# Optimization experiments

Measured on AMD Instinct MI355X. Metric: run time of the kernel, lower is better.

The kernel has to match this reference:

```python
import jax, jax.numpy as jnp
import numpy as np

NHEAD = 8
TEMP = 1.0
LAMB = 1.0
G_MIN = 1e-3


def _linear(x, w, b):
    # torch nn.Linear convention: w is (out, in)
    return x @ w.T + b


def _ln(x, s, b):
    m = x.mean(-1, keepdims=True)
    v = ((x - m) ** 2).mean(-1, keepdims=True)
    return (x - m) / jnp.sqrt(v + 1e-5) * s + b


def _gate(x, w, b):
    # UncertaintyGate, gate_mode='mu_times_evi'
    nig = _linear(x, w, b)  # [B, L, 4]
    mu = nig[..., 0]
    v = jax.nn.softplus(nig[..., 1]) + 1e-6
    alpha = jax.nn.softplus(nig[..., 2]) + 1.0 + 1e-6
    beta = jax.nn.softplus(nig[..., 3]) + 1e-6
    sigma_e2 = beta / (v * (alpha - 1.0))
    g = jax.nn.sigmoid(mu) * jnp.exp(-LAMB * sigma_e2)
    return jnp.clip(g, G_MIN, 1.0)  # [B, L]


def _cross_attn(q, k, v, gate, mask):
    B, Lq, D = q.shape
    Lk = k.shape[1]
    hd = D // NHEAD
    q = q.reshape(B, Lq, NHEAD, hd).transpose(0, 2, 1, 3)
    k = k.reshape(B, Lk, NHEAD, hd).transpose(0, 2, 1, 3)
    v = v.reshape(B, Lk, NHEAD, hd).transpose(0, 2, 1, 3)
    scores = jnp.einsum('bhqd,bhkd->bhqk', q, k) / jnp.sqrt(jnp.float32(hd))
    scores = scores + jnp.log(gate + 1e-9)[:, None, None, :]  # per-key log-gate bias
    scores = jnp.where(mask[:, None, None, :] == 0, -1e9, scores)
    attn = jax.nn.softmax(scores / TEMP, axis=-1)
    out = jnp.einsum('bhqk,bhkd->bhqd', attn, v)
    return out.transpose(0, 2, 1, 3).reshape(B, Lq, D)


def _ffn(x, w1, b1, w2, b2):
    return _linear(jax.nn.gelu(_linear(x, w1, b1), approximate=False), w2, b2)


def setup_inputs() -> dict:
    key = jax.random.key(0)
    ks = iter(jax.random.split(key, 64))
    D, B, Ld, Lp = 512, 16, 256, 1024
    def w(shape, s=0.02):
        return jax.random.normal(next(ks), shape, jnp.float32) * s
    inp = {
        'h_d': jax.random.normal(next(ks), (B, Ld, D), jnp.float32),
        'h_p': jax.random.normal(next(ks), (B, Lp, D), jnp.float32),
        'gd_w': w((4, D)), 'gd_b': jnp.zeros((4,), jnp.float32),
        'gp_w': w((4, D)), 'gp_b': jnp.zeros((4,), jnp.float32),
        'wqd_w': w((D, D)), 'wqd_b': jnp.zeros((D,), jnp.float32),
        'wkp_w': w((D, D)), 'wkp_b': jnp.zeros((D,), jnp.float32),
        'wvp_w': w((D, D)), 'wvp_b': jnp.zeros((D,), jnp.float32),
        'wqp_w': w((D, D)), 'wqp_b': jnp.zeros((D,), jnp.float32),
        'wkd_w': w((D, D)), 'wkd_b': jnp.zeros((D,), jnp.float32),
        'wvd_w': w((D, D)), 'wvd_b': jnp.zeros((D,), jnp.float32),
        'od_w': w((D, D)), 'od_b': jnp.zeros((D,), jnp.float32),
        'op_w': w((D, D)), 'op_b': jnp.zeros((D,), jnp.float32),
        'fd1_w': w((4 * D, D)), 'fd1_b': jnp.zeros((4 * D,), jnp.float32),
        'fd2_w': w((D, 4 * D)), 'fd2_b': jnp.zeros((D,), jnp.float32),
        'fp1_w': w((4 * D, D)), 'fp1_b': jnp.zeros((4 * D,), jnp.float32),
        'fp2_w': w((D, 4 * D)), 'fp2_b': jnp.zeros((D,), jnp.float32),
        'nd1_s': jnp.ones((D,), jnp.float32), 'nd1_b': jnp.zeros((D,), jnp.float32),
        'nd2_s': jnp.ones((D,), jnp.float32), 'nd2_b': jnp.zeros((D,), jnp.float32),
        'np1_s': jnp.ones((D,), jnp.float32), 'np1_b': jnp.zeros((D,), jnp.float32),
        'np2_s': jnp.ones((D,), jnp.float32), 'np2_b': jnp.zeros((D,), jnp.float32),
        'mask_d': jnp.ones((B, Ld), jnp.int32),
        'mask_p': jnp.ones((B, Lp), jnp.int32),
    }
    return inp


def reference(h_d, h_p, gd_w, gd_b, gp_w, gp_b, wqd_w, wqd_b, wkp_w, wkp_b,
              wvp_w, wvp_b, wqp_w, wqp_b, wkd_w, wkd_b, wvd_w, wvd_b,
              od_w, od_b, op_w, op_b, fd1_w, fd1_b, fd2_w, fd2_b,
              fp1_w, fp1_b, fp2_w, fp2_b, nd1_s, nd1_b, nd2_s, nd2_b,
              np1_s, np1_b, np2_s, np2_b, mask_d, mask_p):
    # gates are computed from the ORIGINAL inputs
    g_d = _gate(h_d, gd_w, gd_b)
    g_p = _gate(h_p, gp_w, gp_b)
    # drug attends to protein
    attn_d = _cross_attn(_linear(h_d, wqd_w, wqd_b),
                         _linear(h_p, wkp_w, wkp_b),
                         _linear(h_p, wvp_w, wvp_b), g_p, mask_p)
    h_d = _ln(h_d + _linear(attn_d, od_w, od_b), nd1_s, nd1_b)
    # protein attends to UPDATED drug (matches original control flow)
    attn_p = _cross_attn(_linear(h_p, wqp_w, wqp_b),
                         _linear(h_d, wkd_w, wkd_b),
                         _linear(h_d, wvd_w, wvd_b), g_d, mask_d)
    h_p = _ln(h_p + _linear(attn_p, op_w, op_b), np1_s, np1_b)
    h_d = _ln(h_d + _ffn(h_d, fd1_w, fd1_b, fd2_w, fd2_b), nd2_s, nd2_b)
    h_p = _ln(h_p + _ffn(h_p, fp1_w, fp1_b, fp2_w, fp2_b), np2_s, np2_b)
    return (h_d, h_p)
```

## Files before the change

### kernel.cpp

```cpp
#include <hip/hip_runtime.h>

typedef float f32x4 __attribute__((ext_vector_type(4)));
typedef short bfrag __attribute__((ext_vector_type(8)));
typedef short s16x8 __attribute__((ext_vector_type(8)));
typedef unsigned short u16;

__device__ __forceinline__ u16 f2bf(float f) {
  union { float f; unsigned u; } x; x.f = f;
  unsigned r = x.u + 0x7fffu + ((x.u >> 16) & 1u);
  return (u16)(r >> 16);
}
__device__ __forceinline__ float bf2f(u16 v) {
  union { unsigned u; float f; } x; x.u = ((unsigned)v) << 16;
  return x.f;
}

__device__ __forceinline__ void g2l16(const void* g, void* l) {
  void* gnc = const_cast<void*>(g);
  __builtin_amdgcn_global_load_lds((__attribute__((address_space(1))) void*)gnc,
                                   (__attribute__((address_space(3))) void*)l, 16, 0, 0);
}

__device__ __forceinline__ f32x4 mfma16(bfrag a, bfrag b, f32x4 c) {
  asm volatile("v_mfma_f32_16x16x32_bf16 %0, %1, %2, %0" : "+v"(c) : "v"(a), "v"(b));
  return c;
}

__device__ __forceinline__ float wred_sum(float s) {
  #pragma unroll
  for (int o = 32; o; o >>= 1) s += __shfl_xor(s, o);
  return s;
}

struct CvtArgs {
  const float* s[14];
  u16* d[14];
  int eb[14];
};

__global__ __launch_bounds__(256) void cvt_all(CvtArgs a) {
  const int blk = blockIdx.x;
  int base = 0;
  const float* sp = a.s[0];
  u16* dp = a.d[0];
  #pragma unroll
  for (int i = 0; i < 13; ++i) {
    if (blk >= a.eb[i]) { base = a.eb[i]; sp = a.s[i + 1]; dp = a.d[i + 1]; }
  }
  const size_t gi = ((size_t)(blk - base) * 256 + threadIdx.x) * 4;
  float4 f = *(const float4*)(sp + gi);
  ushort4 o;
  o.x = f2bf(f.x); o.y = f2bf(f.y); o.z = f2bf(f.z); o.w = f2bf(f.w);
  *(ushort4*)(dp + gi) = o;
}

__device__ __forceinline__ float softplus_s(float x) {
  return fmaxf(x, 0.f) + log1pf(expf(-fabsf(x)));
}

__global__ __launch_bounds__(256) void gate_k(
    const float* __restrict__ hd, const float* __restrict__ hp,
    const float* __restrict__ wd, const float* __restrict__ bd,
    const float* __restrict__ wp, const float* __restrict__ bp,
    float* __restrict__ lgd, float* __restrict__ lgp, int mdTok) {
  const int lane = threadIdx.x & 63, wv = threadIdx.x >> 6;
  size_t tok = (size_t)blockIdx.x * 4 + wv;
  const float* h; const float* w4; const float* b4; float* lg;
  if (tok < (size_t)mdTok) { h = hd; w4 = wd; b4 = bd; lg = lgd; }
  else { h = hp; w4 = wp; b4 = bp; lg = lgp; tok -= mdTok; }
  const float* x = h + tok * 512;
  float s0 = 0.f, s1 = 0.f, s2 = 0.f, s3 = 0.f;
  #pragma unroll
  for (int i = 0; i < 8; ++i) {
    int c = (i << 6) + lane;
    float xv = x[c];
    s0 += xv * w4[c];
    s1 += xv * w4[512 + c];
    s2 += xv * w4[1024 + c];
    s3 += xv * w4[1536 + c];
  }
  s0 = wred_sum(s0); s1 = wred_sum(s1); s2 = wred_sum(s2); s3 = wred_sum(s3);
  if (lane == 0) {
    float mu = s0 + b4[0];
    float va = softplus_s(s1 + b4[1]) + 1e-6f;
    float al = softplus_s(s2 + b4[2]) + 1.f + 1e-6f;
    float be = softplus_s(s3 + b4[3]) + 1e-6f;
    float se2 = be / (va * (al - 1.f));
    float g = (1.f / (1.f + expf(-mu))) * expf(-se2);
    g = fminf(fmaxf(g, 1e-3f), 1.f);
    lg[tok] = logf(g + 1e-9f);
  }
}

template <int RES, int OUT>
__global__ __launch_bounds__(256) void ln_k(const void* __restrict__ resv,
                                            const u16* __restrict__ y,
                                            const float* __restrict__ sc,
                                            const float* __restrict__ bi,
                                            void* __restrict__ outv) {
  const int lane = threadIdx.x & 63, w = threadIdx.x >> 6;
  const size_t row = (size_t)blockIdx.x * 4 + w;
  const int c0 = lane * 8;
  float v[8];
  s16x8 yv = *(const s16x8*)(y + row * 512 + c0);
  if constexpr (RES == 0) {
    const float* rf = (const float*)resv + row * 512 + c0;
    float4 r0 = *(const float4*)rf, r1 = *(const float4*)(rf + 4);
    v[0] = r0.x; v[1] = r0.y; v[2] = r0.z; v[3] = r0.w;
    v[4] = r1.x; v[5] = r1.y; v[6] = r1.z; v[7] = r1.w;
  } else {
    s16x8 rv = *(const s16x8*)((const u16*)resv + row * 512 + c0);
    #pragma unroll
    for (int i = 0; i < 8; ++i) v[i] = bf2f((u16)rv[i]);
  }
  float s = 0.f;
  #pragma unroll
  for (int i = 0; i < 8; ++i) { v[i] += bf2f((u16)yv[i]); s += v[i]; }
  s = wred_sum(s);
  float m = s * (1.f / 512.f);
  float s2 = 0.f;
  #pragma unroll
  for (int i = 0; i < 8; ++i) { float d = v[i] - m; s2 += d * d; }
  s2 = wred_sum(s2);
  float inv = rsqrtf(s2 * (1.f / 512.f) + 1e-5f);
  float4 sc0 = *(const float4*)(sc + c0), sc1 = *(const float4*)(sc + c0 + 4);
  float4 bi0 = *(const float4*)(bi + c0), bi1 = *(const float4*)(bi + c0 + 4);
  float scv[8] = {sc0.x, sc0.y, sc0.z, sc0.w, sc1.x, sc1.y, sc1.z, sc1.w};
  float biv[8] = {bi0.x, bi0.y, bi0.z, bi0.w, bi1.x, bi1.y, bi1.z, bi1.w};
  float o[8];
  #pragma unroll
  for (int i = 0; i < 8; ++i) o[i] = (v[i] - m) * inv * scv[i] + biv[i];
  if constexpr (OUT == 0) {
    float* of = (float*)outv + row * 512 + c0;
    *(float4*)of = float4{o[0], o[1], o[2], o[3]};
    *(float4*)(of + 4) = float4{o[4], o[5], o[6], o[7]};
  } else {
    s16x8 ov;
    #pragma unroll
    for (int i = 0; i < 8; ++i) ov[i] = (short)f2bf(o[i]);
    *(s16x8*)((u16*)outv + row * 512 + c0) = ov;
  }
}

template <int KT>
__global__ __launch_bounds__(256) void flash_k(
    const u16* __restrict__ Q, const u16* __restrict__ Kv,
    const u16* __restrict__ Vt, const float* __restrict__ logg,
    const int* __restrict__ mask, u16* __restrict__ Out,
    int Lq, int Lk, float scale) {
  __shared__ __align__(16) u16 Kl[KT * 64];
  __shared__ __align__(16) u16 Vl[64 * KT];
  __shared__ __align__(16) u16 Pl[64 * (KT + 8)];
  const int tid = threadIdx.x;
  const int lane = tid & 63, wv = tid >> 6;
  const int lr = lane & 15, lg4 = lane >> 4;
  const int bh = blockIdx.z;
  const int b = bh >> 3, h = bh & 7;
  const int q0 = blockIdx.x * 64;

  bfrag af[2];
  {
    const u16* qrow = Q + (size_t)(b * Lq + q0 + wv * 16 + lr) * 512 + h * 64;
    af[0] = *(const bfrag*)(qrow + lg4 * 8);
    af[1] = *(const bfrag*)(qrow + 32 + lg4 * 8);
  }
  float mreg[4] = {-3e38f, -3e38f, -3e38f, -3e38f};
  float lreg[4] = {0.f, 0.f, 0.f, 0.f};
  f32x4 Oa[4] = {};
  const float* lgb = logg + (size_t)b * Lk;
  const int* mkb = mask + (size_t)b * Lk;

  const int NKT = Lk / KT;
  for (int t = 0; t < NKT; ++t) {
    const int k0 = t * KT;
    __syncthreads();
    {
      const char* kb = (const char*)(Kv + (size_t)(b * Lk + k0) * 512 + h * 64);
      #pragma unroll
      for (int r = 0; r < KT / 32; ++r) {
        int o = r * 4096 + tid * 16;
        int rr = o >> 7, cd = (o >> 4) & 7;
        int cs = cd ^ (rr & 7);
        g2l16(kb + (size_t)rr * 1024 + cs * 16, (char*)Kl + o);
      }
      const char* vb = (const char*)(Vt + (size_t)bh * 64 * Lk + k0);
      #pragma unroll
      for (int r = 0; r < KT / 32; ++r) {
        int o = r * 4096 + tid * 16;
        int rr = o >> 8, cd = (o >> 4) & 15;
        int cs = (cd & 8) | ((cd & 7) ^ (rr & 7));
        g2l16(vb + (size_t)rr * (Lk * 2) + cs * 16, (char*)Vl + o);
      }
    }
    __syncthreads();

    f32x4 sa[KT / 16];
    #pragma unroll
    for (int n = 0; n < KT / 16; ++n) {
      sa[n] = f32x4{0.f, 0.f, 0.f, 0.f};
      int row = n * 16 + lr;
      #pragma unroll
      for (int ks = 0; ks < 2; ++ks) {
        bfrag kf = *(const bfrag*)(Kl + row * 64 + (((ks * 4 + lg4) ^ (row & 7)) * 8));
        sa[n] = mfma16(af[ks], kf, sa[n]);
      }
    }
    asm volatile("s_nop 7\n\ts_nop 7");

    float pv[KT / 16][4];
    float nm[4] = {-3e38f, -3e38f, -3e38f, -3e38f};
    #pragma unroll
    for (int n = 0; n < KT / 16; ++n) {
      int kk = k0 + n * 16 + lr;
      float lgv = lgb[kk];
      int mkv = mkb[kk];
      #pragma unroll
      for (int e = 0; e < 4; ++e) {
        float tv = mkv ? fmaf(sa[n][e], scale, lgv) : -1e9f;
        pv[n][e] = tv;
        nm[e] = fmaxf(nm[e], tv);
      }
    }
    float fac[4], rs[4];
    #pragma unroll
    for (int e = 0; e < 4; ++e) {
      nm[e] = fmaxf(nm[e], __shfl_xor(nm[e], 1));
      nm[e] = fmaxf(nm[e], __shfl_xor(nm[e], 2));
      nm[e] = fmaxf(nm[e], __shfl_xor(nm[e], 4));
      nm[e] = fmaxf(nm[e], __shfl_xor(nm[e], 8));
      nm[e] = fmaxf(nm[e], mreg[e]);
      fac[e] = __expf(mreg[e] - nm[e]);
      mreg[e] = nm[e];
      rs[e] = 0.f;
    }
    #pragma unroll
    for (int n = 0; n < KT / 16; ++n)
      #pragma unroll
      for (int e = 0; e < 4; ++e) {
        float p = __expf(pv[n][e] - nm[e]);
        pv[n][e] = p;
        rs[e] += p;
      }
    #pragma unroll
    for (int e = 0; e < 4; ++e) {
      rs[e] += __shfl_xor(rs[e], 1);
      rs[e] += __shfl_xor(rs[e], 2);
      rs[e] += __shfl_xor(rs[e], 4);
      rs[e] += __shfl_xor(rs[e], 8);
      lreg[e] = lreg[e] * fac[e] + rs[e];
    }
    #pragma unroll
    for (int n2 = 0; n2 < 4; ++n2)
      #pragma unroll
      for (int e = 0; e < 4; ++e) Oa[n2][e] *= fac[e];

    {
      int prow = wv * 16 + lg4 * 4;
      #pragma unroll
      for (int n = 0; n < KT / 16; ++n)
        #pragma unroll
        for (int e = 0; e < 4; ++e)
          Pl[(prow + e) * (KT + 8) + n * 16 + lr] = f2bf(pv[n][e]);
    }
    #pragma unroll
    for (int ks = 0; ks < KT / 32; ++ks) {
      bfrag pf = *(const bfrag*)(Pl + (wv * 16 + lr) * (KT + 8) + (ks * 4 + lg4) * 8);
      #pragma unroll
      for (int n2 = 0; n2 < 4; ++n2) {
        int vrow = n2 * 16 + lr;
        int ch = ks * 4 + lg4;
        int chs = (ch & 8) | ((ch & 7) ^ (vrow & 7));
        bfrag vf = *(const bfrag*)(Vl + vrow * KT + chs * 8);
        Oa[n2] = mfma16(pf, vf, Oa[n2]);
      }
    }
  }
  asm volatile("s_nop 7\n\ts_nop 7");

  float inv[4];
  #pragma unroll
  for (int e = 0; e < 4; ++e) inv[e] = 1.f / lreg[e];
  u16* ob = Out + (size_t)(b * Lq + q0 + wv * 16 + lg4 * 4) * 512 + h * 64;
  #pragma unroll
  for (int n2 = 0; n2 < 4; ++n2)
    #pragma unroll
    for (int e = 0; e < 4; ++e)
      ob[(size_t)e * 512 + n2 * 16 + lr] = f2bf(Oa[n2][e] * inv[e]);
}

template <int FM, int FN, int EPI>
__global__ __launch_bounds__(256) void gemm_k(
    const u16* __restrict__ A, const u16* __restrict__ W,
    const float* __restrict__ bias, void* __restrict__ C,
    int K, int lda, int ldw, int ldc, int MB, int TR) {
  constexpr int BM = 2 * FM * 16;
  constexpr int BN = 2 * FN * 16;
  __shared__ __align__(16) u16 Al[2][BM * 64];
  __shared__ __align__(16) u16 Wl[2][BN * 64];
  const int tid = threadIdx.x;
  const int qq = gridDim.x >> 3;
  const int wg = (blockIdx.x & 7) * qq + (blockIdx.x >> 3);
  const int by = wg % MB, bx = wg / MB;
  const int row0 = by * BM, col0 = bx * BN;
  const int lane = tid & 63, wv = tid >> 6;
  const int wr = wv >> 1, wc = wv & 1;
  const int rowW = wr * FM * 16, colW = wc * FN * 16;
  const int lr = lane & 15, lg4 = lane >> 4;

  f32x4 acc[FM][FN] = {};
  const int NT = K >> 6;

  auto stage = [&](int bsel, int k0) {
    #pragma unroll
    for (int r = 0; r < BM / 32; ++r) {
      int o = r * 4096 + tid * 16;
      int arow = o >> 7, cd = (o >> 4) & 7, cs = cd ^ (arow & 7);
      g2l16((const char*)(A + (size_t)(row0 + arow) * lda + k0) + cs * 16,
            (char*)Al[bsel] + o);
    }
    #pragma unroll
    for (int r = 0; r < BN / 32; ++r) {
      int o = r * 4096 + tid * 16;
      int wrow = o >> 7, cd = (o >> 4) & 7, cs = cd ^ (wrow & 7);
      g2l16((const char*)(W + (size_t)(col0 + wrow) * ldw + k0) + cs * 16,
            (char*)Wl[bsel] + o);
    }
  };

  auto body = [&](int cur, int t) {
    if (t + 1 < NT) stage(cur ^ 1, (t + 1) << 6);
    bfrag af[FM][2], wf[FN][2];
    #pragma unroll
    for (int m = 0; m < FM; ++m) {
      int rowi = rowW + m * 16 + lr;
      #pragma unroll
      for (int ks = 0; ks < 2; ++ks)
        af[m][ks] =
            *(const bfrag*)(Al[cur] + rowi * 64 + (((ks * 4 + lg4) ^ (rowi & 7)) * 8));
    }
    #pragma unroll
    for (int n = 0; n < FN; ++n) {
      int rowi = colW + n * 16 + lr;
      #pragma unroll
      for (int ks = 0; ks < 2; ++ks)
        wf[n][ks] =
            *(const bfrag*)(Wl[cur] + rowi * 64 + (((ks * 4 + lg4) ^ (rowi & 7)) * 8));
    }
    #pragma unroll
    for (int m = 0; m < FM; ++m)
      #pragma unroll
      for (int n = 0; n < FN; ++n) {
        acc[m][n] = mfma16(af[m][0], wf[n][0], acc[m][n]);
        acc[m][n] = mfma16(af[m][1], wf[n][1], acc[m][n]);
      }
    __syncthreads();
  };

  stage(0, 0);
  __syncthreads();
  for (int t = 0; t < NT; t += 2) {
    body(0, t);
    body(1, t + 1);
  }
  asm volatile("s_nop 7\n\ts_nop 7\n\ts_nop 7");

  #pragma unroll
  for (int m = 0; m < FM; ++m) {
    #pragma unroll
    for (int n = 0; n < FN; ++n) {
      int rb = row0 + rowW + m * 16 + lg4 * 4;
      int c = col0 + colW + n * 16 + lr;
      float bv = bias[c];
      if constexpr (EPI == 1) {
        u16* Cu = (u16*)C;
        #pragma unroll
        for (int e = 0; e < 4; ++e)
          Cu[(size_t)(rb + e) * ldc + c] = f2bf(acc[m][n][e] + bv);
      } else if constexpr (EPI == 2) {
        u16* Cu = (u16*)C;
        #pragma unroll
        for (int e = 0; e < 4; ++e) {
          float vv = acc[m][n][e] + bv;
          float gl = 0.5f * vv * (1.f + erff(vv * 0.70710678118f));
          Cu[(size_t)(rb + e) * ldc + c] = f2bf(gl);
        }
      } else {
        u16* Cu = (u16*)C;
        int b2 = rb / TR, j0 = rb - b2 * TR;
        int h2 = c >> 6, dd = c & 63;
        ushort4 pk;
        pk.x = f2bf(acc[m][n][0] + bv);
        pk.y = f2bf(acc[m][n][1] + bv);
        pk.z = f2bf(acc[m][n][2] + bv);
        pk.w = f2bf(acc[m][n][3] + bv);
        *(ushort4*)&Cu[(((size_t)b2 * 8 + h2) * 64 + dd) * TR + j0] = pk;
      }
    }
  }
}

extern "C" void kernel_launch(void* const* d_in, const int* in_sizes, int n_in,
                              void* d_out, int out_size, void* d_ws, size_t ws_size,
                              hipStream_t stream) {
  const float* h_d = (const float*)d_in[0];
  const float* h_p = (const float*)d_in[1];
  const float* gd_w = (const float*)d_in[2];
  const float* gd_b = (const float*)d_in[3];
  const float* gp_w = (const float*)d_in[4];
  const float* gp_b = (const float*)d_in[5];
  const float* wqd_w = (const float*)d_in[6];  const float* wqd_b = (const float*)d_in[7];
  const float* wkp_w = (const float*)d_in[8];  const float* wkp_b = (const float*)d_in[9];
  const float* wvp_w = (const float*)d_in[10]; const float* wvp_b = (const float*)d_in[11];
  const float* wqp_w = (const float*)d_in[12]; const float* wqp_b = (const float*)d_in[13];
  const float* wkd_w = (const float*)d_in[14]; const float* wkd_b = (const float*)d_in[15];
  const float* wvd_w = (const float*)d_in[16]; const float* wvd_b = (const float*)d_in[17];
  const float* od_w = (const float*)d_in[18];  const float* od_b = (const float*)d_in[19];
  const float* op_w = (const float*)d_in[20];  const float* op_b = (const float*)d_in[21];
  const float* fd1_w = (const float*)d_in[22]; const float* fd1_b = (const float*)d_in[23];
  const float* fd2_w = (const float*)d_in[24]; const float* fd2_b = (const float*)d_in[25];
  const float* fp1_w = (const float*)d_in[26]; const float* fp1_b = (const float*)d_in[27];
  const float* fp2_w = (const float*)d_in[28]; const float* fp2_b = (const float*)d_in[29];
  const float* nd1_s = (const float*)d_in[30]; const float* nd1_b = (const float*)d_in[31];
  const float* nd2_s = (const float*)d_in[32]; const float* nd2_b = (const float*)d_in[33];
  const float* np1_s = (const float*)d_in[34]; const float* np1_b = (const float*)d_in[35];
  const float* np2_s = (const float*)d_in[36]; const float* np2_b = (const float*)d_in[37];
  const int* mask_d = (const int*)d_in[38];
  const int* mask_p = (const int*)d_in[39];

  constexpr int B = 16, Ld = 256, Lp = 1024, D = 512, H = 8, F = 2048;
  constexpr int Md = B * Ld;
  constexpr int Mp = B * Lp;
  constexpr int BH = B * H;

  char* ws = (char*)d_ws;
  size_t off = 0;
  auto alloc = [&](size_t bytes) {
    size_t o = off;
    off += (bytes + 255) & ~(size_t)255;
    return o;
  };
  auto a16 = [&](size_t els) { return (u16*)(ws + alloc(els * 2)); };
  auto a32 = [&](size_t els) { return (float*)(ws + alloc(els * 4)); };

  u16* w_qd = a16((size_t)D * D);
  u16* w_kp = a16((size_t)D * D);
  u16* w_vp = a16((size_t)D * D);
  u16* w_qp = a16((size_t)D * D);
  u16* w_kd = a16((size_t)D * D);
  u16* w_vd = a16((size_t)D * D);
  u16* w_od = a16((size_t)D * D);
  u16* w_op = a16((size_t)D * D);
  u16* w_fd1 = a16((size_t)F * D);
  u16* w_fd2 = a16((size_t)F * D);
  u16* w_fp1 = a16((size_t)F * D);
  u16* w_fp2 = a16((size_t)F * D);

  u16* hd16 = a16((size_t)Md * D);
  u16* hd2_16 = a16((size_t)Md * D);
  u16* hp16 = a16((size_t)Mp * D);
  u16* qd16 = a16((size_t)Md * D);
  u16* kp16 = a16((size_t)Mp * D);
  u16* vt16 = a16((size_t)Mp * D);
  u16* obuf16 = a16((size_t)Mp * D);
  u16* t16 = a16((size_t)Mp * F);
  float* logg_d = a32(Md);
  float* logg_p = a32(Mp);

  {
    CvtArgs a;
    const float* src[14] = {h_d, h_p, wqd_w, wkp_w, wvp_w, wqp_w, wkd_w,
                            wvd_w, od_w, op_w, fd1_w, fd2_w, fp1_w, fp2_w};
    u16* dst[14] = {hd16, hp16, w_qd, w_kp, w_vp, w_qp, w_kd,
                    w_vd, w_od, w_op, w_fd1, w_fd2, w_fp1, w_fp2};
    const int nelem[14] = {Md * D, Mp * D, D * D, D * D, D * D, D * D, D * D,
                           D * D, D * D, D * D, F * D, F * D, F * D, F * D};
    int pfx = 0;
    for (int i = 0; i < 14; ++i) {
      a.s[i] = src[i];
      a.d[i] = dst[i];
      pfx += nelem[i] / 1024;
      a.eb[i] = pfx;
    }
    cvt_all<<<pfx, 256, 0, stream>>>(a);
  }

  gate_k<<<(Md + Mp) / 4, 256, 0, stream>>>(h_d, h_p, gd_w, gd_b, gp_w, gp_b,
                                            logg_d, logg_p, Md);

  gemm_k<4, 4, 1><<<(Md / 128) * (D / 128), 256, 0, stream>>>(
      hd16, w_qd, wqd_b, qd16, D, D, D, D, Md / 128, 0);
  gemm_k<4, 4, 1><<<(Mp / 128) * (D / 128), 256, 0, stream>>>(
      hp16, w_kp, wkp_b, kp16, D, D, D, D, Mp / 128, 0);
  gemm_k<4, 4, 3><<<(Mp / 128) * (D / 128), 256, 0, stream>>>(
      hp16, w_vp, wvp_b, vt16, D, D, D, 0, Mp / 128, Lp);

  flash_k<128><<<dim3(Ld / 64, 1, BH), 256, 0, stream>>>(
      qd16, kp16, vt16, logg_p, mask_p, hd16, Ld, Lp, 0.125f);

  gemm_k<4, 4, 1><<<(Md / 128) * (D / 128), 256, 0, stream>>>(
      hd16, w_od, od_b, obuf16, D, D, D, D, Md / 128, 0);
  ln_k<0, 1><<<Md / 4, 256, 0, stream>>>(h_d, obuf16, nd1_s, nd1_b, hd2_16);

  gemm_k<4, 4, 1><<<(Mp / 128) * (D / 128), 256, 0, stream>>>(
      hp16, w_qp, wqp_b, kp16, D, D, D, D, Mp / 128, 0);
  gemm_k<4, 4, 1><<<(Md / 128) * (D / 128), 256, 0, stream>>>(
      hd2_16, w_kd, wkd_b, qd16, D, D, D, D, Md / 128, 0);
  gemm_k<4, 4, 3><<<(Md / 128) * (D / 128), 256, 0, stream>>>(
      hd2_16, w_vd, wvd_b, vt16, D, D, D, 0, Md / 128, Ld);

  flash_k<128><<<dim3(Lp / 64, 1, BH), 256, 0, stream>>>(
      kp16, qd16, vt16, logg_d, mask_d, hp16, Lp, Ld, 0.125f);

  gemm_k<4, 4, 1><<<(Mp / 128) * (D / 128), 256, 0, stream>>>(
      hp16, w_op, op_b, obuf16, D, D, D, D, Mp / 128, 0);
  ln_k<0, 1><<<Mp / 4, 256, 0, stream>>>(h_p, obuf16, np1_s, np1_b, hp16);

  gemm_k<4, 4, 2><<<(Md / 128) * (F / 128), 256, 0, stream>>>(
      hd2_16, w_fd1, fd1_b, t16, D, D, D, F, Md / 128, 0);
  gemm_k<4, 4, 1><<<(Md / 128) * (D / 128), 256, 0, stream>>>(
      t16, w_fd2, fd2_b, obuf16, F, F, F, D, Md / 128, 0);
  ln_k<1, 0><<<Md / 4, 256, 0, stream>>>(hd2_16, obuf16, nd2_s, nd2_b, (float*)d_out);

  gemm_k<4, 4, 2><<<(Mp / 128) * (F / 128), 256, 0, stream>>>(
      hp16, w_fp1, fp1_b, t16, D, D, D, F, Mp / 128, 0);
  gemm_k<4, 4, 1><<<(Mp / 128) * (D / 128), 256, 0, stream>>>(
      t16, w_fp2, fp2_b, obuf16, F, F, F, D, Mp / 128, 0);
  ln_k<1, 0><<<Mp / 4, 256, 0, stream>>>(hp16, obuf16, np2_s, np2_b,
                                         (float*)d_out + (size_t)Md * D);
}
```

Before: 406.6 us.

## Pipeline GEMM loads with explicit vmcnt waits and column-major tile order

The GEMM main loop is rewritten as a single double-buffered loop. It stages the next K tile, then uses a partial s_waitcnt vmcnt(8) and raw s_barrier in place of __syncthreads. This lets the next tile's global-to-LDS loads stay in flight while the current tile is consumed, and fragments are now loaded per k-substep to lower register pressure. The workgroup-to-tile mapping also changes so consecutive workgroups walk along N instead of M, which changes L2 reuse of A rows versus W columns. The hand-counted vmcnt value depends on the number of loads per stage (8 for FM=FN=4), so the code breaks silently if the tile configuration changes.

```diff
diff --git a/kernel.cpp b/kernel.cpp
--- a/kernel.cpp
+++ b/kernel.cpp
@@ -292,7 +292,7 @@
 __global__ __launch_bounds__(256) void gemm_k(
     const u16* __restrict__ A, const u16* __restrict__ W,
     const float* __restrict__ bias, void* __restrict__ C,
-    int K, int lda, int ldw, int ldc, int MB, int TR) {
+    int K, int lda, int ldw, int ldc, int NB, int TR) {
   constexpr int BM = 2 * FM * 16;
   constexpr int BN = 2 * FN * 16;
   __shared__ __align__(16) u16 Al[2][BM * 64];
@@ -300,7 +300,7 @@
   const int tid = threadIdx.x;
   const int qq = gridDim.x >> 3;
   const int wg = (blockIdx.x & 7) * qq + (blockIdx.x >> 3);
-  const int by = wg % MB, bx = wg / MB;
+  const int bx = wg % NB, by = wg / NB;
   const int row0 = by * BM, col0 = bx * BN;
   const int lane = tid & 63, wv = tid >> 6;
   const int wr = wv >> 1, wc = wv & 1;
@@ -327,40 +327,38 @@
     }
   };
 
-  auto body = [&](int cur, int t) {
-    if (t + 1 < NT) stage(cur ^ 1, (t + 1) << 6);
-    bfrag af[FM][2], wf[FN][2];
-    #pragma unroll
-    for (int m = 0; m < FM; ++m) {
-      int rowi = rowW + m * 16 + lr;
-      #pragma unroll
-      for (int ks = 0; ks < 2; ++ks)
-        af[m][ks] =
+  stage(0, 0);
+  int cur = 0;
+  for (int t = 0; t < NT; ++t) {
+    if (t + 1 < NT) {
+      stage(cur ^ 1, (t + 1) << 6);
+      asm volatile("s_waitcnt vmcnt(8)" ::: "memory");
+    } else {
+      asm volatile("s_waitcnt vmcnt(0)" ::: "memory");
+    }
+    asm volatile("s_barrier" ::: "memory");
+    #pragma unroll
+    for (int ks = 0; ks < 2; ++ks) {
+      bfrag af[FM], wf[FN];
+      #pragma unroll
+      for (int m = 0; m < FM; ++m) {
+        int rowi = rowW + m * 16 + lr;
+        af[m] =
             *(const bfrag*)(Al[cur] + rowi * 64 + (((ks * 4 + lg4) ^ (rowi & 7)) * 8));
-    }
-    #pragma unroll
-    for (int n = 0; n < FN; ++n) {
-      int rowi = colW + n * 16 + lr;
-      #pragma unroll
-      for (int ks = 0; ks < 2; ++ks)
-        wf[n][ks] =
+      }
+      #pragma unroll
+      for (int n = 0; n < FN; ++n) {
+        int rowi = colW + n * 16 + lr;
+        wf[n] =
             *(const bfrag*)(Wl[cur] + rowi * 64 + (((ks * 4 + lg4) ^ (rowi & 7)) * 8));
-    }
-    #pragma unroll
-    for (int m = 0; m < FM; ++m)
-      #pragma unroll
-      for (int n = 0; n < FN; ++n) {
-        acc[m][n] = mfma16(af[m][0], wf[n][0], acc[m][n]);
-        acc[m][n] = mfma16(af[m][1], wf[n][1], acc[m][n]);
-      }
-    __syncthreads();
-  };
-
-  stage(0, 0);
-  __syncthreads();
-  for (int t = 0; t < NT; t += 2) {
-    body(0, t);
-    body(1, t + 1);
+      }
+      #pragma unroll
+      for (int m = 0; m < FM; ++m)
+        #pragma unroll
+        for (int n = 0; n < FN; ++n) acc[m][n] = mfma16(af[m], wf[n], acc[m][n]);
+    }
+    asm volatile("s_barrier" ::: "memory");
+    cur ^= 1;
   }
   asm volatile("s_nop 7\n\ts_nop 7\n\ts_nop 7");
 
@@ -488,43 +486,43 @@
                                             logg_d, logg_p, Md);
 
   gemm_k<4, 4, 1><<<(Md / 128) * (D / 128), 256, 0, stream>>>(
-      hd16, w_qd, wqd_b, qd16, D, D, D, D, Md / 128, 0);
+      hd16, w_qd, wqd_b, qd16, D, D, D, D, D / 128, 0);
   gemm_k<4, 4, 1><<<(Mp / 128) * (D / 128), 256, 0, stream>>>(
-      hp16, w_kp, wkp_b, kp16, D, D, D, D, Mp / 128, 0);
+      hp16, w_kp, wkp_b, kp16, D, D, D, D, D / 128, 0);
   gemm_k<4, 4, 3><<<(Mp / 128) * (D / 128), 256, 0, stream>>>(
-      hp16, w_vp, wvp_b, vt16, D, D, D, 0, Mp / 128, Lp);
+      hp16, w_vp, wvp_b, vt16, D, D, D, 0, D / 128, Lp);
 
   flash_k<128><<<dim3(Ld / 64, 1, BH), 256, 0, stream>>>(
       qd16, kp16, vt16, logg_p, mask_p, hd16, Ld, Lp, 0.125f);
 
   gemm_k<4, 4, 1><<<(Md / 128) * (D / 128), 256, 0, stream>>>(
-      hd16, w_od, od_b, obuf16, D, D, D, D, Md / 128, 0);
+      hd16, w_od, od_b, obuf16, D, D, D, D, D / 128, 0);
   ln_k<0, 1><<<Md / 4, 256, 0, stream>>>(h_d, obuf16, nd1_s, nd1_b, hd2_16);
 
   gemm_k<4, 4, 1><<<(Mp / 128) * (D / 128), 256, 0, stream>>>(
-      hp16, w_qp, wqp_b, kp16, D, D, D, D, Mp / 128, 0);
+      hp16, w_qp, wqp_b, kp16, D, D, D, D, D / 128, 0);
   gemm_k<4, 4, 1><<<(Md / 128) * (D / 128), 256, 0, stream>>>(
-      hd2_16, w_kd, wkd_b, qd16, D, D, D, D, Md / 128, 0);
+      hd2_16, w_kd, wkd_b, qd16, D, D, D, D, D / 128, 0);
   gemm_k<4, 4, 3><<<(Md / 128) * (D / 128), 256, 0, stream>>>(
-      hd2_16, w_vd, wvd_b, vt16, D, D, D, 0, Md / 128, Ld);
+      hd2_16, w_vd, wvd_b, vt16, D, D, D, 0, D / 128, Ld);
 
   flash_k<128><<<dim3(Lp / 64, 1, BH), 256, 0, stream>>>(
       kp16, qd16, vt16, logg_d, mask_d, hp16, Lp, Ld, 0.125f);
 
   gemm_k<4, 4, 1><<<(Mp / 128) * (D / 128), 256, 0, stream>>>(
-      hp16, w_op, op_b, obuf16, D, D, D, D, Mp / 128, 0);
+      hp16, w_op, op_b, obuf16, D, D, D, D, D / 128, 0);
   ln_k<0, 1><<<Mp / 4, 256, 0, stream>>>(h_p, obuf16, np1_s, np1_b, hp16);
 
   gemm_k<4, 4, 2><<<(Md / 128) * (F / 128), 256, 0, stream>>>(
-      hd2_16, w_fd1, fd1_b, t16, D, D, D, F, Md / 128, 0);
+      hd2_16, w_fd1, fd1_b, t16, D, D, D, F, F / 128, 0);
   gemm_k<4, 4, 1><<<(Md / 128) * (D / 128), 256, 0, stream>>>(
-      t16, w_fd2, fd2_b, obuf16, F, F, F, D, Md / 128, 0);
+      t16, w_fd2, fd2_b, obuf16, F, F, F, D, D / 128, 0);
   ln_k<1, 0><<<Md / 4, 256, 0, stream>>>(hd2_16, obuf16, nd2_s, nd2_b, (float*)d_out);
 
   gemm_k<4, 4, 2><<<(Mp / 128) * (F / 128), 256, 0, stream>>>(
-      hp16, w_fp1, fp1_b, t16, D, D, D, F, Mp / 128, 0);
+      hp16, w_fp1, fp1_b, t16, D, D, D, F, F / 128, 0);
   gemm_k<4, 4, 1><<<(Mp / 128) * (D / 128), 256, 0, stream>>>(
-      t16, w_fp2, fp2_b, obuf16, F, F, F, D, Mp / 128, 0);
+      t16, w_fp2, fp2_b, obuf16, F, F, F, D, D / 128, 0);
   ln_k<1, 0><<<Mp / 4, 256, 0, stream>>>(hp16, obuf16, np2_s, np2_b,
                                          (float*)d_out + (size_t)Md * D);
 }
```

Result: faster. 394.5 us (-3.0%).
